# Performance work log

Hardware: AMD Instinct MI355X
Metric: run time of the kernel (lower is better)

Reference implementation:

```python
import jax, jax.numpy as jnp
import numpy as np

N = 50000       # nodes
E = 1600000     # edges (avg degree 32)
IN = 128        # node_in_dim
D = 64          # node_out_dim (= GRU hidden)
H = 1           # heads
ED = 3          # edge_in_dim
STEPS = 3       # num_step_message_passing
EPS = 1e-5      # BatchNorm eps
SLOPE = 0.2     # LeakyReLU negative slope (GAT default)


def setup_inputs() -> dict:
    key = jax.random.key(0)
    ks = jax.random.split(key, 16)
    s_in = 1.0 / np.sqrt(IN)
    s_d = 1.0 / np.sqrt(D)
    return {
        "x": jax.random.normal(ks[0], (N, IN), jnp.float32),
        "edge_attr": jax.random.normal(ks[1], (E, ED), jnp.float32),
        "mlp_w": jax.random.normal(ks[2], (IN, D), jnp.float32) * s_in,
        "mlp_b": jnp.zeros((D,), jnp.float32),
        "bn_g": jnp.ones((D,), jnp.float32),
        "bn_b": jnp.zeros((D,), jnp.float32),
        "conv_w": jax.random.normal(ks[3], (D, H * D), jnp.float32) * s_d,
        "att_dst": jax.random.normal(ks[4], (H, D), jnp.float32) * s_d,
        "att_src": jax.random.normal(ks[5], (H, D), jnp.float32) * s_d,
        "att_edge": jax.random.normal(ks[6], (H, ED), jnp.float32) * s_d,
        "w_ih": jax.random.normal(ks[7], (3 * D, H * D), jnp.float32) * s_d,
        "w_hh": jax.random.normal(ks[8], (3 * D, D), jnp.float32) * s_d,
        "b_ih": jnp.zeros((3 * D,), jnp.float32),
        "b_hh": jnp.zeros((3 * D,), jnp.float32),
        "lin_w": jax.random.normal(ks[9], (IN, D), jnp.float32) * s_in,
        "lin_b": jnp.zeros((D,), jnp.float32),
        "edge_index": jax.random.randint(ks[10], (2, E), 0, N, jnp.int64),
    }


def _egat_conv(out, edge_attr, src, dst, conv_w, att_dst, att_src, att_edge):
    # out: [N, D] -> xt: [N, H, D]
    xt = (out @ conv_w).reshape(N, H, D)
    # per-node attention halves (avoid gathering twice): [N, H]
    a_dst_n = jnp.einsum("nhd,hd->nh", xt, att_dst)
    a_src_n = jnp.einsum("nhd,hd->nh", xt, att_src)
    # per-edge logits: [E, H]
    logits = a_dst_n[dst] + a_src_n[src] + edge_attr @ att_edge.T
    logits = jnp.where(logits >= 0, logits, SLOPE * logits)
    # segment softmax over destination nodes
    seg_max = jax.ops.segment_max(logits, dst, num_segments=N)  # [N, H]
    seg_max = jnp.where(jnp.isfinite(seg_max), seg_max, 0.0)
    expd = jnp.exp(logits - seg_max[dst])
    denom = jax.ops.segment_sum(expd, dst, num_segments=N)      # [N, H]
    alpha = expd / denom[dst]                                   # [E, H]
    # attention-weighted aggregation of source features
    msgs = alpha[:, :, None] * xt[src]                          # [E, H, D]
    agg = jax.ops.segment_sum(msgs, dst, num_segments=N)        # [N, H, D]
    return agg.reshape(N, H * D)


def _gru_cell(x_in, h, w_ih, w_hh, b_ih, b_hh):
    gi = x_in @ w_ih.T + b_ih
    gh = h @ w_hh.T + b_hh
    gi_r, gi_z, gi_n = jnp.split(gi, 3, axis=-1)
    gh_r, gh_z, gh_n = jnp.split(gh, 3, axis=-1)
    r = jax.nn.sigmoid(gi_r + gh_r)
    z = jax.nn.sigmoid(gi_z + gh_z)
    n = jnp.tanh(gi_n + r * gh_n)
    return (1.0 - z) * n + z * h


def reference(x, edge_attr, mlp_w, mlp_b, bn_g, bn_b, conv_w, att_dst,
              att_src, att_edge, w_ih, w_hh, b_ih, b_hh, lin_w, lin_b,
              edge_index):
    src, dst = edge_index[0], edge_index[1]
    # initial embedding: ReLU(BatchNorm(Linear(x))) with batch stats
    h0 = x @ mlp_w + mlp_b
    mu = jnp.mean(h0, axis=0)
    var = jnp.var(h0, axis=0)
    out = jax.nn.relu((h0 - mu) * jax.lax.rsqrt(var + EPS) * bn_g + bn_b)
    h = out
    for _ in range(STEPS):
        m = jax.nn.relu(_egat_conv(out, edge_attr, src, dst,
                                   conv_w, att_dst, att_src, att_edge))
        h = _gru_cell(m, h, w_ih, w_hh, b_ih, b_hh)
        out = h
    return x @ lin_w + lin_b + out
```

## Files before the change

kernel.cpp:

```cpp
#include <hip/hip_runtime.h>

typedef unsigned short ushort_t;
typedef unsigned int uint_t;
typedef __attribute__((ext_vector_type(8))) short bf16x8;
typedef __attribute__((ext_vector_type(4))) float f32x4;

#define N_NODES 50000
#define N_EDGES 1600000
#define NB_BKT 391
#define CAP_BKT 4608
#define CAP_B 6144
#define GBK 391

__device__ __forceinline__ float bfu(ushort_t u) {
    return __uint_as_float(((uint_t)u) << 16);
}
__device__ __forceinline__ ushort_t f2b(float f) {
    uint_t x = __float_as_uint(f);
    uint_t r = (x + 0x7FFFu + ((x >> 16) & 1u)) >> 16;
    return (ushort_t)r;
}
__device__ __forceinline__ float sigm(float x) {
    return 1.0f / (1.0f + __expf(-x));
}
__device__ __forceinline__ float tanh_f(float x) {
    return 1.0f - 2.0f / (__expf(2.0f * x) + 1.0f);
}
__device__ __forceinline__ bf16x8 pack8(const float* v) {
    bf16x8 r;
#pragma unroll
    for (int j = 0; j < 8; ++j) r[j] = (short)f2b(v[j]);
    return r;
}
__device__ __forceinline__ int ld_src(const int* __restrict__ ei, int i, int f64) {
    return f64 ? ei[2 * i] : ei[i];
}
__device__ __forceinline__ int ld_dst(const int* __restrict__ ei, int i, int f64) {
    return f64 ? ei[2 * N_EDGES + 2 * i] : ei[N_EDGES + i];
}
__device__ __forceinline__ bool is_f64(const int* flag) { return flag[0] > 2048; }

__global__ void k_sentinel(float* __restrict__ out, int n) {
    int i = blockIdx.x * 256 + threadIdx.x;
    if (i < n) out[i] = 100.0f;
}

__global__ void k_prep(const float* __restrict__ w_ih, const float* __restrict__ w_hh,
                       const float* __restrict__ conv_w, const float* __restrict__ mlp_w,
                       const float* __restrict__ lin_w, const int* __restrict__ ei,
                       ushort_t* __restrict__ wb, ushort_t* __restrict__ cwb,
                       ushort_t* __restrict__ mlpT, ushort_t* __restrict__ linT,
                       int* __restrict__ flag, int* __restrict__ gtail) {
    int blk = blockIdx.x;
    if (blk < 176) {
        int t = blk * 256 + threadIdx.x;
        if (t < 24576) {
            const float* w = (t < 12288) ? w_ih : w_hh;
            wb[t] = f2b(w[t < 12288 ? t : t - 12288]);
        } else if (t < 28672) {
            int r = t - 24576;
            int j = r >> 6, k = r & 63;
            cwb[j * 64 + k] = f2b(conv_w[k * 64 + j]);
        } else if (t < 36864) {
            int r = t - 28672;
            int j = r >> 7, k = r & 127;
            mlpT[j * 128 + k] = f2b(mlp_w[k * 64 + j]);
        } else if (t < 45056) {
            int r = t - 36864;
            int j = r >> 7, k = r & 127;
            linT[j * 128 + k] = f2b(lin_w[k * 64 + j]);
        }
    } else if (blk == 176) {
        __shared__ int red[256];
        int tid = threadIdx.x;
        int zeros = 0;
#pragma unroll
        for (int j = 0; j < 16; ++j) {
            int slot = (tid * 16 + j) * 2 + 1;
            if (ei[slot] == 0) zeros++;
        }
        red[tid] = zeros;
        __syncthreads();
        for (int off = 128; off; off >>= 1) {
            if (tid < off) red[tid] += red[tid + off];
            __syncthreads();
        }
        if (tid == 0) flag[0] = red[0];
    } else {
        int b = (blk - 177) * 256 + threadIdx.x;
        if (b < NB_BKT) gtail[b] = b * CAP_BKT;
    }
}

__global__ __launch_bounds__(256) void k_embbkt(
    const int* __restrict__ ei, const int* __restrict__ flag,
    const float* __restrict__ ea, const float* __restrict__ ae,
    int* __restrict__ gtail, uint2* __restrict__ bkt, int e,
    const float* __restrict__ x, const ushort_t* __restrict__ mlpT,
    const float* __restrict__ mlp_b, float* __restrict__ h0, int n) {
    if (blockIdx.x < GBK) {
        __shared__ int cnt[NB_BKT];
        __shared__ int gbase[NB_BKT];
        for (int i = threadIdx.x; i < NB_BKT; i += 256) cnt[i] = 0;
        __syncthreads();
        int base = blockIdx.x * 4096;
        int f64 = is_f64(flag);
        float a0 = ae[0], a1 = ae[1], a2 = ae[2];
        uint_t w0[16], w1[16];
        int bk[16], rk[16];
#pragma unroll
        for (int j = 0; j < 16; ++j) {
            int i = base + j * 256 + threadIdx.x;
            bk[j] = -1;
            if (i < e) {
                int d = ld_dst(ei, i, f64);
                if ((uint_t)d < (uint_t)N_NODES) {
                    int s = ld_src(ei, i, f64);
                    if ((uint_t)s >= (uint_t)N_NODES) s = 0;
                    float ed = ea[i * 3] * a0 + ea[i * 3 + 1] * a1 + ea[i * 3 + 2] * a2;
                    bk[j] = d >> 7;
                    w0[j] = (uint_t)s | ((uint_t)(d & 127) << 16);
                    w1[j] = __float_as_uint(ed);
                    rk[j] = atomicAdd(&cnt[bk[j]], 1);
                }
            }
        }
        __syncthreads();
        for (int t = threadIdx.x; t < NB_BKT; t += 256) {
            int c = cnt[t];
            gbase[t] = c ? atomicAdd(&gtail[t], c) : 0;
        }
        __syncthreads();
#pragma unroll
        for (int j = 0; j < 16; ++j) {
            if (bk[j] >= 0) {
                int pos = gbase[bk[j]] + rk[j];
                if (pos < (bk[j] + 1) * CAP_BKT) {
                    uint2 p;
                    p.x = w0[j];
                    p.y = w1[j];
                    bkt[pos] = p;
                }
            }
        }
    } else {
        int lane = threadIdx.x & 63;
        int wv = threadIdx.x >> 6;
        int tile = (blockIdx.x - GBK) * 4 + wv;
        if (tile * 16 >= n) return;
        int nb16 = tile * 16;
        int mrow = lane & 15, q = lane >> 4;
        const float* xp = x + (nb16 + mrow) * 128 + q * 8;
        bf16x8 a[4];
#pragma unroll
        for (int kc = 0; kc < 4; ++kc) {
            float hv[8];
            const float* p = xp + kc * 32;
#pragma unroll
            for (int j = 0; j < 8; ++j) hv[j] = p[j];
            a[kc] = pack8(hv);
        }
        f32x4 acc[4];
#pragma unroll
        for (int t = 0; t < 4; ++t) acc[t] = (f32x4){0.f, 0.f, 0.f, 0.f};
#pragma unroll
        for (int kc = 0; kc < 4; ++kc) {
#pragma unroll
            for (int t = 0; t < 4; ++t) {
                bf16x8 b =
                    *(const bf16x8*)(mlpT + (t * 16 + mrow) * 128 + kc * 32 + q * 8);
                acc[t] = __builtin_amdgcn_mfma_f32_16x16x32_bf16(a[kc], b, acc[t], 0, 0, 0);
            }
        }
#pragma unroll
        for (int t = 0; t < 4; ++t) {
            int j = t * 16 + mrow;
            float bias = mlp_b[j];
#pragma unroll
            for (int r = 0; r < 4; ++r)
                h0[(nb16 + q * 4 + r) * 64 + j] = acc[t][r] + bias;
        }
    }
}

__global__ __launch_bounds__(256) void k_statsort(
    const int* __restrict__ gtail, const uint2* __restrict__ bkt,
    uint_t* __restrict__ pk, int* __restrict__ rs, int n,
    const float* __restrict__ h0, float* __restrict__ stats) {
    __shared__ char smem[26624];
    int tid = threadIdx.x;
    if (blockIdx.x < NB_BKT) {
        int* red = (int*)smem;
        int* cnt = (int*)(smem + 1024);
        int* sc = (int*)(smem + 1536);
        uint_t* stg = (uint_t*)(smem + 2048);
        int b = blockIdx.x;
        int partial = 0;
        for (int i = tid; i < b; i += 256)
            partial += min(gtail[i] - i * CAP_BKT, CAP_BKT);
        red[tid] = partial;
        __syncthreads();
        for (int off = 128; off; off >>= 1) {
            if (tid < off) red[tid] += red[tid + off];
            __syncthreads();
        }
        int obase = red[0];
        int node0 = b * 128;
        int nloc = min(128, n - node0);
        int size = min(gtail[b] - b * CAP_BKT, CAP_BKT);
        const uint2* bin = bkt + b * CAP_BKT;
        for (int i = tid; i < 128; i += 256) cnt[i] = 0;
        __syncthreads();
        for (int ofs = tid; ofs < size; ofs += 256) {
            int dlow = (bin[ofs].x >> 16) & 127;
            atomicAdd(&cnt[dlow], 1);
        }
        __syncthreads();
        if (tid < 128) sc[tid] = cnt[tid];
        __syncthreads();
        for (int off = 1; off < 128; off <<= 1) {
            int add = (tid < 128 && tid >= off) ? sc[tid - off] : 0;
            __syncthreads();
            if (tid < 128) sc[tid] += add;
            __syncthreads();
        }
        if (tid < 128) sc[tid] -= cnt[tid];
        __syncthreads();
        if (tid < nloc) rs[node0 + tid] = obase + sc[tid];
        if (b == NB_BKT - 1 && tid == 0) rs[n] = obase + size;
        for (int i = tid; i < 128; i += 256) cnt[i] = 0;
        __syncthreads();
        for (int ofs = tid; ofs < size; ofs += 256) {
            uint2 p = bin[ofs];
            int dlow = (p.x >> 16) & 127;
            int r = atomicAdd(&cnt[dlow], 1);
            int pos = sc[dlow] + r;
            uint_t q = (p.x & 0xFFFFu) |
                       ((uint_t)f2b(__uint_as_float(p.y)) << 16);
            if (pos < CAP_B) stg[pos] = q;
            else pk[obase + pos] = q;
        }
        __syncthreads();
        int wlim = min(size, CAP_B);
        for (int ofs = tid; ofs < wlim; ofs += 256) pk[obase + ofs] = stg[ofs];
    } else {
        float* ssum = (float*)smem;
        float* ssq = (float*)(smem + 1024);
        int gid = (blockIdx.x - NB_BKT) * 256 + tid;
        int col = gid & 63;
        int rg = gid >> 6;
        float s = 0.f, s2 = 0.f;
        for (int row = rg; row < n; row += 1024) {
            float v = h0[row * 64 + col];
            s += v;
            s2 += v * v;
        }
        ssum[tid] = s;
        ssq[tid] = s2;
        __syncthreads();
        if (tid < 64) {
            s = ssum[tid] + ssum[tid + 64] + ssum[tid + 128] + ssum[tid + 192];
            s2 = ssq[tid] + ssq[tid + 64] + ssq[tid + 128] + ssq[tid + 192];
            atomicAdd(&stats[tid], s);
            atomicAdd(&stats[64 + tid], s2);
        }
    }
}

__global__ __launch_bounds__(256) void k_xt(float* __restrict__ h,
                                            const ushort_t* __restrict__ cwb,
                                            const float* __restrict__ att_dst,
                                            const float* __restrict__ att_src,
                                            const float* __restrict__ bn_g,
                                            const float* __restrict__ bn_b,
                                            const float* __restrict__ stats,
                                            float inv_n, int apply,
                                            ushort_t* __restrict__ xt,
                                            float* __restrict__ adst,
                                            float* __restrict__ asrc, int n) {
    __shared__ float scb[64], shb[64];
    if (apply) {
        int tid = threadIdx.x;
        if (tid < 64) {
            float mu = stats[tid] * inv_n;
            float var = fmaxf(stats[64 + tid] * inv_n - mu * mu, 0.f);
            float sc = rsqrtf(var + 1e-5f) * bn_g[tid];
            scb[tid] = sc;
            shb[tid] = bn_b[tid] - mu * sc;
        }
        __syncthreads();
    }
    int lane = threadIdx.x & 63;
    int wv = threadIdx.x >> 6;
    int tile = blockIdx.x * 4 + wv;
    if (tile * 16 >= n) return;
    int nb16 = tile * 16;
    int mrow = lane & 15, q = lane >> 4;
    bf16x8 ah[2];
    {
        float* hp = h + (nb16 + mrow) * 64 + q * 8;
        float hv[8];
#pragma unroll
        for (int kh = 0; kh < 2; ++kh) {
            float* p = hp + kh * 32;
#pragma unroll
            for (int j = 0; j < 8; ++j) hv[j] = p[j];
            if (apply) {
                int cb = kh * 32 + q * 8;
#pragma unroll
                for (int j = 0; j < 8; ++j) {
                    hv[j] = fmaxf(hv[j] * scb[cb + j] + shb[cb + j], 0.f);
                    p[j] = hv[j];
                }
            }
            ah[kh] = pack8(hv);
        }
    }
    f32x4 acc[4];
#pragma unroll
    for (int t = 0; t < 4; ++t) acc[t] = (f32x4){0.f, 0.f, 0.f, 0.f};
#pragma unroll
    for (int kh = 0; kh < 2; ++kh) {
#pragma unroll
        for (int t = 0; t < 4; ++t) {
            bf16x8 b = *(const bf16x8*)(cwb + (t * 16 + mrow) * 64 + kh * 32 + q * 8);
            acc[t] = __builtin_amdgcn_mfma_f32_16x16x32_bf16(ah[kh], b, acc[t], 0, 0, 0);
        }
    }
    float sd[4] = {0, 0, 0, 0}, ss[4] = {0, 0, 0, 0};
#pragma unroll
    for (int t = 0; t < 4; ++t) {
        int j = t * 16 + mrow;
        float ad = att_dst[j], as = att_src[j];
#pragma unroll
        for (int r = 0; r < 4; ++r) {
            float v = acc[t][r];
            xt[(nb16 + q * 4 + r) * 64 + j] = f2b(v);
            sd[r] += v * ad;
            ss[r] += v * as;
        }
    }
#pragma unroll
    for (int off = 1; off < 16; off <<= 1) {
#pragma unroll
        for (int r = 0; r < 4; ++r) {
            sd[r] += __shfl_xor(sd[r], off);
            ss[r] += __shfl_xor(ss[r], off);
        }
    }
    if (mrow == 0) {
#pragma unroll
        for (int r = 0; r < 4; ++r) {
            adst[nb16 + q * 4 + r] = sd[r];
            asrc[nb16 + q * 4 + r] = ss[r];
        }
    }
}

__global__ __launch_bounds__(256) void k_agg(const int* __restrict__ rs,
                                             const uint_t* __restrict__ pk,
                                             const float* __restrict__ adst,
                                             const float* __restrict__ asrc,
                                             const ushort_t* __restrict__ xt,
                                             ushort_t* __restrict__ m, int n) {
    __shared__ float s_w[4][64];
    __shared__ int s_s[4][64];
    int lane = threadIdx.x & 63;
    int wv = threadIdx.x >> 6;
    int v = blockIdx.x * 4 + wv;
    if (v >= n) return;
    int start = rs[v], end = rs[v + 1];
    if (start >= end) {
        m[v * 64 + lane] = 0;
        return;
    }
    float adv = adst[v];
    int g = lane >> 3;
    int cb = (lane & 7) * 8;
    float acc[8] = {0, 0, 0, 0, 0, 0, 0, 0};
    float dsum = 0.f;
    for (int base = start; base < end; base += 64) {
        int e = base + lane;
        float w = 0.f;
        int s = 0;
        if (e < end) {
            uint_t p = pk[e];
            s = (int)(p & 0xFFFFu);
            float l = adv + asrc[s] + bfu((ushort_t)(p >> 16));
            l = (l >= 0.f) ? l : 0.2f * l;
            w = __expf(l);
        }
        dsum += w;
        s_w[wv][lane] = w;
        s_s[wv][lane] = s;
        int cnt = min(64, end - base);
        int nb8 = (cnt + 7) >> 3;
        for (int tb = 0; tb < nb8; ++tb) {
            int sl = tb * 8 + g;
            float w8 = s_w[wv][sl];
            int s8 = s_s[wv][sl];
            uint4 qv = *(const uint4*)(xt + s8 * 64 + cb);
            acc[0] += w8 * __uint_as_float(qv.x << 16);
            acc[1] += w8 * __uint_as_float(qv.x & 0xFFFF0000u);
            acc[2] += w8 * __uint_as_float(qv.y << 16);
            acc[3] += w8 * __uint_as_float(qv.y & 0xFFFF0000u);
            acc[4] += w8 * __uint_as_float(qv.z << 16);
            acc[5] += w8 * __uint_as_float(qv.z & 0xFFFF0000u);
            acc[6] += w8 * __uint_as_float(qv.w << 16);
            acc[7] += w8 * __uint_as_float(qv.w & 0xFFFF0000u);
        }
    }
#pragma unroll
    for (int off = 32; off; off >>= 1) dsum += __shfl_xor(dsum, off);
#pragma unroll
    for (int off = 8; off < 64; off <<= 1) {
#pragma unroll
        for (int j = 0; j < 8; ++j) acc[j] += __shfl_xor(acc[j], off);
    }
    float inv = 1.0f / fmaxf(dsum, 1e-20f);
    if (g == 0) {
        uint4 o;
        o.x = (uint_t)f2b(fmaxf(acc[0] * inv, 0.f)) |
              ((uint_t)f2b(fmaxf(acc[1] * inv, 0.f)) << 16);
        o.y = (uint_t)f2b(fmaxf(acc[2] * inv, 0.f)) |
              ((uint_t)f2b(fmaxf(acc[3] * inv, 0.f)) << 16);
        o.z = (uint_t)f2b(fmaxf(acc[4] * inv, 0.f)) |
              ((uint_t)f2b(fmaxf(acc[5] * inv, 0.f)) << 16);
        o.w = (uint_t)f2b(fmaxf(acc[6] * inv, 0.f)) |
              ((uint_t)f2b(fmaxf(acc[7] * inv, 0.f)) << 16);
        *(uint4*)(m + v * 64 + cb) = o;
    }
}

__global__ __launch_bounds__(256) void k_gru(const ushort_t* __restrict__ mb,
                                             float* __restrict__ h,
                                             const ushort_t* __restrict__ wb,
                                             const float* __restrict__ b_ih,
                                             const float* __restrict__ b_hh, int n) {
    int lane = threadIdx.x & 63;
    int wv = threadIdx.x >> 6;
    int tile = blockIdx.x * 4 + wv;
    if (tile * 16 >= n) return;
    int nb16 = tile * 16;
    int mrow = lane & 15, q = lane >> 4;
    bf16x8 am[2], ah[2];
    {
        const ushort_t* mp = mb + (nb16 + mrow) * 64 + q * 8;
        am[0] = *(const bf16x8*)(mp);
        am[1] = *(const bf16x8*)(mp + 32);
        const float* hp = h + (nb16 + mrow) * 64 + q * 8;
        float hv[8];
#pragma unroll
        for (int j = 0; j < 8; ++j) hv[j] = hp[j];
        ah[0] = pack8(hv);
#pragma unroll
        for (int j = 0; j < 8; ++j) hv[j] = hp[32 + j];
        ah[1] = pack8(hv);
    }
    f32x4 acc[24];
#pragma unroll
    for (int t = 0; t < 24; ++t) acc[t] = (f32x4){0.f, 0.f, 0.f, 0.f};
#pragma unroll
    for (int kh = 0; kh < 2; ++kh) {
#pragma unroll
        for (int t = 0; t < 12; ++t) {
            bf16x8 b = *(const bf16x8*)(wb + (t * 16 + mrow) * 64 + kh * 32 + q * 8);
            acc[t] = __builtin_amdgcn_mfma_f32_16x16x32_bf16(am[kh], b, acc[t], 0, 0, 0);
        }
#pragma unroll
        for (int t = 0; t < 12; ++t) {
            bf16x8 b =
                *(const bf16x8*)(wb + (192 + t * 16 + mrow) * 64 + kh * 32 + q * 8);
            acc[12 + t] =
                __builtin_amdgcn_mfma_f32_16x16x32_bf16(ah[kh], b, acc[12 + t], 0, 0, 0);
        }
    }
#pragma unroll
    for (int t = 0; t < 4; ++t) {
        int j = t * 16 + mrow;
        float bir = b_ih[j], biz = b_ih[64 + j], bin = b_ih[128 + j];
        float bhr = b_hh[j], bhz = b_hh[64 + j], bhn = b_hh[128 + j];
#pragma unroll
        for (int r = 0; r < 4; ++r) {
            int node = nb16 + q * 4 + r;
            float gr = acc[t][r] + bir + acc[12 + t][r] + bhr;
            float gz = acc[4 + t][r] + biz + acc[16 + t][r] + bhz;
            float rr = sigm(gr);
            float zz = sigm(gz);
            float tt = acc[8 + t][r] + bin + rr * (acc[20 + t][r] + bhn);
            float hp = h[node * 64 + j];
            h[node * 64 + j] = (1.f - zz) * tanh_f(tt) + zz * hp;
        }
    }
}

__global__ __launch_bounds__(256) void k_out(const float* __restrict__ x,
                                             const ushort_t* __restrict__ linT,
                                             const float* __restrict__ lin_b,
                                             const float* __restrict__ h,
                                             float* __restrict__ out, int n) {
    int lane = threadIdx.x & 63;
    int wv = threadIdx.x >> 6;
    int tile = blockIdx.x * 4 + wv;
    if (tile * 16 >= n) return;
    int nb16 = tile * 16;
    int mrow = lane & 15, q = lane >> 4;
    const float* xp = x + (nb16 + mrow) * 128 + q * 8;
    bf16x8 a[4];
#pragma unroll
    for (int kc = 0; kc < 4; ++kc) {
        float hv[8];
        const float* p = xp + kc * 32;
#pragma unroll
        for (int j = 0; j < 8; ++j) hv[j] = p[j];
        a[kc] = pack8(hv);
    }
    f32x4 acc[4];
#pragma unroll
    for (int t = 0; t < 4; ++t) acc[t] = (f32x4){0.f, 0.f, 0.f, 0.f};
#pragma unroll
    for (int kc = 0; kc < 4; ++kc) {
#pragma unroll
        for (int t = 0; t < 4; ++t) {
            bf16x8 b = *(const bf16x8*)(linT + (t * 16 + mrow) * 128 + kc * 32 + q * 8);
            acc[t] = __builtin_amdgcn_mfma_f32_16x16x32_bf16(a[kc], b, acc[t], 0, 0, 0);
        }
    }
#pragma unroll
    for (int t = 0; t < 4; ++t) {
        int j = t * 16 + mrow;
        float bias = lin_b[j];
#pragma unroll
        for (int r = 0; r < 4; ++r) {
            int node = nb16 + q * 4 + r;
            out[node * 64 + j] = acc[t][r] + bias + h[node * 64 + j];
        }
    }
}

extern "C" void kernel_launch(void* const* d_in, const int* in_sizes, int n_in,
                              void* d_out, int out_size, void* d_ws, size_t ws_size,
                              hipStream_t stream) {
    const float* x = (const float*)d_in[0];
    const float* edge_attr = (const float*)d_in[1];
    const float* mlp_w = (const float*)d_in[2];
    const float* mlp_b = (const float*)d_in[3];
    const float* bn_g = (const float*)d_in[4];
    const float* bn_b = (const float*)d_in[5];
    const float* conv_w = (const float*)d_in[6];
    const float* att_dst = (const float*)d_in[7];
    const float* att_src = (const float*)d_in[8];
    const float* att_edge = (const float*)d_in[9];
    const float* w_ih = (const float*)d_in[10];
    const float* w_hh = (const float*)d_in[11];
    const float* b_ih = (const float*)d_in[12];
    const float* b_hh = (const float*)d_in[13];
    const float* lin_w = (const float*)d_in[14];
    const float* lin_b = (const float*)d_in[15];
    const int* ei = (const int*)d_in[16];

    char* ws = (char*)d_ws;
    float* f_h = (float*)(ws + 0);
    ushort_t* mb = (ushort_t*)(ws + 12800000);
    ushort_t* xt = (ushort_t*)(ws + 19200000);
    uint2* bkt = (uint2*)(ws + 25600000);
    uint_t* pk = (uint_t*)(ws + 40013824);
    float* f_adst = (float*)(ws + 46413824);
    float* f_asrc = (float*)(ws + 46614016);
    int* row_start = (int*)(ws + 46814208);
    float* stats = (float*)(ws + 47014656);
    int* flag = (int*)(ws + 47015168);
    ushort_t* wb = (ushort_t*)(ws + 47015680);
    ushort_t* cwb = (ushort_t*)(ws + 47064832);
    ushort_t* mlpT = (ushort_t*)(ws + 47073024);
    ushort_t* linT = (ushort_t*)(ws + 47089408);
    int* gtail = (int*)(ws + 47105792);

    const size_t needed = 47107840;
    if (ws_size < needed) {
        k_sentinel<<<(out_size + 255) / 256, 256, 0, stream>>>((float*)d_out, out_size);
        return;
    }

    const int n = N_NODES, e = N_EDGES;
    const int gT = ((n + 15) / 16 + 3) / 4;
    const int gN4 = (n + 3) / 4;
    const int gPrep = 176 + 1 + (NB_BKT + 255) / 256;
    const float inv_n = 1.0f / (float)n;

    hipMemsetAsync(stats, 0, 512, stream);

    k_prep<<<gPrep, 256, 0, stream>>>(w_ih, w_hh, conv_w, mlp_w, lin_w, ei, wb, cwb,
                                      mlpT, linT, flag, gtail);
    k_embbkt<<<GBK + gT, 256, 0, stream>>>(ei, flag, edge_attr, att_edge, gtail, bkt, e,
                                           x, mlpT, mlp_b, f_h, n);
    k_statsort<<<NB_BKT + 256, 256, 0, stream>>>(gtail, bkt, pk, row_start, n, f_h,
                                                 stats);

    for (int s = 0; s < 3; ++s) {
        k_xt<<<gT, 256, 0, stream>>>(f_h, cwb, att_dst, att_src, bn_g, bn_b, stats,
                                     inv_n, s == 0 ? 1 : 0, xt, f_adst, f_asrc, n);
        k_agg<<<gN4, 256, 0, stream>>>(row_start, pk, f_adst, f_asrc, xt, mb, n);
        k_gru<<<gT, 256, 0, stream>>>(mb, f_h, wb, b_ih, b_hh, n);
    }

    k_out<<<gT, 256, 0, stream>>>(x, linT, lin_b, f_h, (float*)d_out, n);
}
```

Before: 403.9 us.

## Fuse next-step xt projection into GRU kernel and stage weights in LDS

The per-step k_xt launch is folded into the GRU kernel: after updating h, each wave re-reads its own tile rows, projects them with conv_w via MFMA, and writes xt plus the attention halves for the next step. Only the first BN-applied projection stays as a separate k_xt. The GRU and conv weights are now copied into padded shared memory per block, replacing repeated global loads, and the previous h values are loaded before the MFMAs. The edge-bucketing grid is also doubled with half the edges per block. Together these cut two kernel launches and one pass over h, at the cost of roughly 64KB of LDS per block, which lowers occupancy, plus a weight-staging prologue in every block.

Result: faster. 370.1 us (-8.4%).

```diff
diff --git a/kernel.cpp b/kernel.cpp
--- a/kernel.cpp
+++ b/kernel.cpp
@@ -10,7 +10,8 @@
 #define NB_BKT 391
 #define CAP_BKT 4608
 #define CAP_B 6144
-#define GBK 391
+#define GBK 782
+#define WPAD 72
 
 __device__ __forceinline__ float bfu(ushort_t u) {
     return __uint_as_float(((uint_t)u) << 16);
@@ -103,13 +104,13 @@
         __shared__ int gbase[NB_BKT];
         for (int i = threadIdx.x; i < NB_BKT; i += 256) cnt[i] = 0;
         __syncthreads();
-        int base = blockIdx.x * 4096;
+        int base = blockIdx.x * 2048;
         int f64 = is_f64(flag);
         float a0 = ae[0], a1 = ae[1], a2 = ae[2];
-        uint_t w0[16], w1[16];
-        int bk[16], rk[16];
-#pragma unroll
-        for (int j = 0; j < 16; ++j) {
+        uint_t w0[8], w1[8];
+        int bk[8], rk[8];
+#pragma unroll
+        for (int j = 0; j < 8; ++j) {
             int i = base + j * 256 + threadIdx.x;
             bk[j] = -1;
             if (i < e) {
@@ -132,7 +133,7 @@
         }
         __syncthreads();
 #pragma unroll
-        for (int j = 0; j < 16; ++j) {
+        for (int j = 0; j < 8; ++j) {
             if (bk[j] >= 0) {
                 int pos = gbase[bk[j]] + rk[j];
                 if (pos < (bk[j] + 1) * CAP_BKT) {
@@ -235,8 +236,7 @@
             int dlow = (p.x >> 16) & 127;
             int r = atomicAdd(&cnt[dlow], 1);
             int pos = sc[dlow] + r;
-            uint_t q = (p.x & 0xFFFFu) |
-                       ((uint_t)f2b(__uint_as_float(p.y)) << 16);
+            uint_t q = (p.x & 0xFFFFu) | ((uint_t)f2b(__uint_as_float(p.y)) << 16);
             if (pos < CAP_B) stg[pos] = q;
             else pk[obase + pos] = q;
         }
@@ -274,12 +274,12 @@
                                             const float* __restrict__ bn_g,
                                             const float* __restrict__ bn_b,
                                             const float* __restrict__ stats,
-                                            float inv_n, int apply,
+                                            float inv_n,
                                             ushort_t* __restrict__ xt,
                                             float* __restrict__ adst,
                                             float* __restrict__ asrc, int n) {
     __shared__ float scb[64], shb[64];
-    if (apply) {
+    {
         int tid = threadIdx.x;
         if (tid < 64) {
             float mu = stats[tid] * inv_n;
@@ -303,15 +303,11 @@
 #pragma unroll
         for (int kh = 0; kh < 2; ++kh) {
             float* p = hp + kh * 32;
-#pragma unroll
-            for (int j = 0; j < 8; ++j) hv[j] = p[j];
-            if (apply) {
-                int cb = kh * 32 + q * 8;
-#pragma unroll
-                for (int j = 0; j < 8; ++j) {
-                    hv[j] = fmaxf(hv[j] * scb[cb + j] + shb[cb + j], 0.f);
-                    p[j] = hv[j];
-                }
+            int cb = kh * 32 + q * 8;
+#pragma unroll
+            for (int j = 0; j < 8; ++j) {
+                hv[j] = fmaxf(p[j] * scb[cb + j] + shb[cb + j], 0.f);
+                p[j] = hv[j];
             }
             ah[kh] = pack8(hv);
         }
@@ -432,29 +428,56 @@
     }
 }
 
-__global__ __launch_bounds__(256) void k_gru(const ushort_t* __restrict__ mb,
-                                             float* __restrict__ h,
-                                             const ushort_t* __restrict__ wb,
-                                             const float* __restrict__ b_ih,
-                                             const float* __restrict__ b_hh, int n) {
+__global__ __launch_bounds__(256) void k_gruxt(
+    const ushort_t* __restrict__ mb, float* __restrict__ h,
+    const ushort_t* __restrict__ wb, const ushort_t* __restrict__ cwb,
+    const float* __restrict__ b_ih, const float* __restrict__ b_hh,
+    const float* __restrict__ att_dst, const float* __restrict__ att_src,
+    int do_xt, ushort_t* __restrict__ xt, float* __restrict__ adst,
+    float* __restrict__ asrc, int n) {
+    __shared__ ushort_t swb[384 * WPAD];
+    __shared__ ushort_t scw[64 * WPAD];
+    {
+        const uint2* src = (const uint2*)wb;
+        for (int g = threadIdx.x; g < 6144; g += 256) {
+            uint2 v = src[g];
+            int row = g >> 4;
+            int col = (g & 15) * 4;
+            *(uint2*)(swb + row * WPAD + col) = v;
+        }
+        const uint2* srcc = (const uint2*)cwb;
+        for (int g = threadIdx.x; g < 1024; g += 256) {
+            uint2 v = srcc[g];
+            int row = g >> 4;
+            int col = (g & 15) * 4;
+            *(uint2*)(scw + row * WPAD + col) = v;
+        }
+    }
+    __syncthreads();
     int lane = threadIdx.x & 63;
     int wv = threadIdx.x >> 6;
     int tile = blockIdx.x * 4 + wv;
     if (tile * 16 >= n) return;
     int nb16 = tile * 16;
     int mrow = lane & 15, q = lane >> 4;
+    float hp[4][4];
+#pragma unroll
+    for (int t = 0; t < 4; ++t)
+#pragma unroll
+        for (int r = 0; r < 4; ++r)
+            hp[t][r] = h[(nb16 + q * 4 + r) * 64 + t * 16 + mrow];
     bf16x8 am[2], ah[2];
     {
         const ushort_t* mp = mb + (nb16 + mrow) * 64 + q * 8;
         am[0] = *(const bf16x8*)(mp);
         am[1] = *(const bf16x8*)(mp + 32);
-        const float* hp = h + (nb16 + mrow) * 64 + q * 8;
+        const float* hpt = h + (nb16 + mrow) * 64 + q * 8;
         float hv[8];
 #pragma unroll
-        for (int j = 0; j < 8; ++j) hv[j] = hp[j];
+        for (int j = 0; j < 8; ++j) hv[j] = hpt[j];
         ah[0] = pack8(hv);
 #pragma unroll
-        for (int j = 0; j < 8; ++j) hv[j] = hp[32 + j];
+        for (int j = 0; j < 8; ++j) hv[j] = hpt[32 + j];
         ah[1] = pack8(hv);
     }
     f32x4 acc[24];
@@ -464,13 +487,13 @@
     for (int kh = 0; kh < 2; ++kh) {
 #pragma unroll
         for (int t = 0; t < 12; ++t) {
-            bf16x8 b = *(const bf16x8*)(wb + (t * 16 + mrow) * 64 + kh * 32 + q * 8);
+            bf16x8 b = *(const bf16x8*)(swb + (t * 16 + mrow) * WPAD + kh * 32 + q * 8);
             acc[t] = __builtin_amdgcn_mfma_f32_16x16x32_bf16(am[kh], b, acc[t], 0, 0, 0);
         }
 #pragma unroll
         for (int t = 0; t < 12; ++t) {
             bf16x8 b =
-                *(const bf16x8*)(wb + (192 + t * 16 + mrow) * 64 + kh * 32 + q * 8);
+                *(const bf16x8*)(swb + (192 + t * 16 + mrow) * WPAD + kh * 32 + q * 8);
             acc[12 + t] =
                 __builtin_amdgcn_mfma_f32_16x16x32_bf16(ah[kh], b, acc[12 + t], 0, 0, 0);
         }
@@ -488,8 +511,59 @@
             float rr = sigm(gr);
             float zz = sigm(gz);
             float tt = acc[8 + t][r] + bin + rr * (acc[20 + t][r] + bhn);
-            float hp = h[node * 64 + j];
-            h[node * 64 + j] = (1.f - zz) * tanh_f(tt) + zz * hp;
+            h[node * 64 + j] = (1.f - zz) * tanh_f(tt) + zz * hp[t][r];
+        }
+    }
+    if (!do_xt) return;
+    __threadfence_block();
+    bf16x8 ah2[2];
+    {
+        const float* hpt = h + (nb16 + mrow) * 64 + q * 8;
+        float hv[8];
+#pragma unroll
+        for (int j = 0; j < 8; ++j) hv[j] = hpt[j];
+        ah2[0] = pack8(hv);
+#pragma unroll
+        for (int j = 0; j < 8; ++j) hv[j] = hpt[32 + j];
+        ah2[1] = pack8(hv);
+    }
+    f32x4 xacc[4];
+#pragma unroll
+    for (int t = 0; t < 4; ++t) xacc[t] = (f32x4){0.f, 0.f, 0.f, 0.f};
+#pragma unroll
+    for (int kh = 0; kh < 2; ++kh) {
+#pragma unroll
+        for (int t = 0; t < 4; ++t) {
+            bf16x8 b = *(const bf16x8*)(scw + (t * 16 + mrow) * WPAD + kh * 32 + q * 8);
+            xacc[t] = __builtin_amdgcn_mfma_f32_16x16x32_bf16(ah2[kh], b, xacc[t], 0, 0, 0);
+        }
+    }
+    float sd[4] = {0, 0, 0, 0}, ss[4] = {0, 0, 0, 0};
+#pragma unroll
+    for (int t = 0; t < 4; ++t) {
+        int j = t * 16 + mrow;
+        float ad = att_dst[j], as = att_src[j];
+#pragma unroll
+        for (int r = 0; r < 4; ++r) {
+            float v = xacc[t][r];
+            xt[(nb16 + q * 4 + r) * 64 + j] = f2b(v);
+            sd[r] += v * ad;
+            ss[r] += v * as;
+        }
+    }
+#pragma unroll
+    for (int off = 1; off < 16; off <<= 1) {
+#pragma unroll
+        for (int r = 0; r < 4; ++r) {
+            sd[r] += __shfl_xor(sd[r], off);
+            ss[r] += __shfl_xor(ss[r], off);
+        }
+    }
+    if (mrow == 0) {
+#pragma unroll
+        for (int r = 0; r < 4; ++r) {
+            adst[nb16 + q * 4 + r] = sd[r];
+            asrc[nb16 + q * 4 + r] = ss[r];
         }
     }
 }
@@ -596,12 +670,13 @@
                                            x, mlpT, mlp_b, f_h, n);
     k_statsort<<<NB_BKT + 256, 256, 0, stream>>>(gtail, bkt, pk, row_start, n, f_h,
                                                  stats);
+    k_xt<<<gT, 256, 0, stream>>>(f_h, cwb, att_dst, att_src, bn_g, bn_b, stats, inv_n,
+                                 xt, f_adst, f_asrc, n);
 
     for (int s = 0; s < 3; ++s) {
-        k_xt<<<gT, 256, 0, stream>>>(f_h, cwb, att_dst, att_src, bn_g, bn_b, stats,
-                                     inv_n, s == 0 ? 1 : 0, xt, f_adst, f_asrc, n);
         k_agg<<<gN4, 256, 0, stream>>>(row_start, pk, f_adst, f_asrc, xt, mb, n);
-        k_gru<<<gT, 256, 0, stream>>>(mb, f_h, wb, b_ih, b_hh, n);
+        k_gruxt<<<gT, 256, 0, stream>>>(mb, f_h, wb, cwb, b_ih, b_hh, att_dst, att_src,
+                                        (s < 2) ? 1 : 0, xt, f_adst, f_asrc, n);
     }
 
     k_out<<<gT, 256, 0, stream>>>(x, linT, lin_b, f_h, (float*)d_out, n);
```
